# Optimization experiments

Measured on AMD Instinct MI355X. Metric: run time of the kernel, lower is better.

Reference implementation:

```python
import jax, jax.numpy as jnp
import numpy as np

B, S, H, NH, G = 2, 2048, 2048, 16, 2
HD = H // NH          # head_dim = 128
NKV = NH // G         # kv heads = 8
EPS = 1e-6


def setup_inputs() -> dict:
    key = jax.random.key(0)
    ks = jax.random.split(key, 5)
    sc = 0.02
    return {
        "x": jax.random.normal(ks[0], (B, S, H), jnp.float32),
        "wq": jax.random.normal(ks[1], (H, H), jnp.float32) * sc,
        "wk": jax.random.normal(ks[2], (H, H // G), jnp.float32) * sc,
        "wv": jax.random.normal(ks[3], (H, H // G), jnp.float32) * sc,
        "wo": jax.random.normal(ks[4], (H, H), jnp.float32) * sc,
        "rms_w": jnp.ones((HD,), jnp.float32),
        "token_positions": jnp.arange(S, dtype=jnp.int32),
    }


def _rmsnorm(x, w):
    # x: (b, s, HD, n_heads); normalize over the head_dim axis (axis 2)
    ms = jnp.mean(x * x, axis=2, keepdims=True)
    return x * jax.lax.rsqrt(ms + EPS) * w[None, None, :, None]


def _rope(x, pos):
    # x: (b, s, HD, n); interleaved-pair rotation along HD, base 10000
    half = HD // 2
    inv_freq = 1.0 / (10000.0 ** (jnp.arange(half, dtype=jnp.float32) * 2.0 / HD))
    ang = pos.astype(jnp.float32)[:, None] * inv_freq[None, :]   # (s, HD/2)
    cos = jnp.cos(ang)[None, :, :, None]
    sin = jnp.sin(ang)[None, :, :, None]
    x1 = x[:, :, 0::2, :]
    x2 = x[:, :, 1::2, :]
    r1 = x1 * cos - x2 * sin
    r2 = x1 * sin + x2 * cos
    return jnp.stack([r1, r2], axis=3).reshape(x.shape)


def reference(x, wq, wk, wv, wo, rms_w, token_positions):
    b, s, _ = x.shape
    # projections, split hidden as (head_dim, n_heads) exactly like the torch .view
    q = (x @ wq).reshape(b, s, HD, NH)
    k = (x @ wk).reshape(b, s, HD, NKV)
    v = (x @ wv).reshape(b, s, HD, NKV)
    # per-head RMSNorm (over head_dim) then RoPE on Q and K
    q = _rope(_rmsnorm(q, rms_w), token_positions)
    k = _rope(_rmsnorm(k, rms_w), token_positions)
    # grouped-query attention: group G query heads per kv head
    q5 = q.reshape(b, s, HD, NKV, G)
    scores = jnp.einsum('bsdkg,btdk->bkgst', q5, k)          # (b,NKV,G,s,s)
    mask = jnp.triu(jnp.ones((s, s), bool), 1)               # causal
    scores = jnp.where(mask[None, None, None], -jnp.inf, scores)
    attn = jax.nn.softmax(scores / jnp.sqrt(jnp.float32(HD)), axis=-1)
    ctx = jnp.einsum('bkgst,btdk->bkgsd', attn, v)           # (b,NKV,G,s,HD)
    ctx = ctx.reshape(b, NH, s, HD).transpose(0, 2, 1, 3).reshape(b, s, H)
    return ctx @ wo
```

## Files before the change

kernel.cpp:

```cpp
#include <hip/hip_runtime.h>
#include <hip/hip_bf16.h>
#include <stdint.h>

typedef unsigned short u16;
typedef uint32_t u32;
typedef __attribute__((ext_vector_type(8))) short s8v;
typedef __attribute__((ext_vector_type(4))) float f4v;
typedef __attribute__((ext_vector_type(4))) unsigned int u4v;

#define SQ   2048
#define HDIM 2048
#define HD_  128
#define NH_  16
#define NKV_ 8

__device__ __forceinline__ u16 f2b(float f) {
  uint32_t u = __builtin_bit_cast(uint32_t, f);
  u += 0x7fffu + ((u >> 16) & 1u);
  return (u16)(u >> 16);
}
__device__ __forceinline__ float b2f(u16 v) {
  uint32_t u = ((uint32_t)v) << 16;
  return __builtin_bit_cast(float, u);
}
__device__ __forceinline__ u32 pk2(float lo, float hi) {
  return (u32)f2b(lo) | ((u32)f2b(hi) << 16);
}
__device__ __forceinline__ u32 cvtpk(float lo, float hi) {
  u32 r;
  asm("v_cvt_pk_bf16_f32 %0, %1, %2" : "=v"(r) : "v"(lo), "v"(hi));
  return r;
}

__global__ __launch_bounds__(256) void k_cast(const float* __restrict__ in,
                                              u16* __restrict__ out, int n4) {
  int i = blockIdx.x * 256 + threadIdx.x;
  if (i >= n4) return;
  f4v v = *(const f4v*)(in + (size_t)i * 4);
  union { u16 s[4]; uint64_t u; } o;
  o.s[0] = f2b(v[0]); o.s[1] = f2b(v[1]); o.s[2] = f2b(v[2]); o.s[3] = f2b(v[3]);
  *(uint64_t*)(out + (size_t)i * 4) = o.u;
}

__global__ __launch_bounds__(256) void k_transpose4(const float* __restrict__ wq,
                                                    const float* __restrict__ wk,
                                                    const float* __restrict__ wv,
                                                    const float* __restrict__ wo,
                                                    u16* __restrict__ wqt,
                                                    u16* __restrict__ wkt,
                                                    u16* __restrict__ wvt,
                                                    u16* __restrict__ wot) {
  const int z = blockIdx.z;
  const float* in = (z == 0) ? wq : (z == 1) ? wk : (z == 2) ? wv : wo;
  u16* out = (z == 0) ? wqt : (z == 1) ? wkt : (z == 2) ? wvt : wot;
  const int cols = (z == 1 || z == 2) ? 1024 : 2048;
  int c0 = blockIdx.x * 32, r0 = blockIdx.y * 32;
  if (c0 >= cols) return;
  __shared__ float tile[32][33];
  int tx = threadIdx.x & 31, ty = threadIdx.x >> 5;
#pragma unroll
  for (int i = 0; i < 32; i += 8)
    tile[ty + i][tx] = in[(size_t)(r0 + ty + i) * cols + c0 + tx];
  __syncthreads();
#pragma unroll
  for (int i = 0; i < 32; i += 8)
    out[(size_t)(c0 + ty + i) * 2048 + r0 + tx] = f2b(tile[tx][ty + i]);
}

template <int F32OUT>
__global__ __launch_bounds__(256) void k_gemm(const u16* __restrict__ A,
                                              const u16* __restrict__ Bt,
                                              void* __restrict__ C,
                                              int M, int N, int K) {
  __shared__ __align__(16) u16 As[128 * 64];
  __shared__ __align__(16) u16 Bs[128 * 64];
  const int tid = threadIdx.x;
  const int lane = tid & 63, wvi = tid >> 6;
  const int wm = wvi >> 1, wn = wvi & 1;
  const int l15 = lane & 15, l4 = lane >> 4;
  const int m0 = blockIdx.y * 128, n0 = blockIdx.x * 128;
  auto* As3 = (__attribute__((address_space(3))) char*)As;
  auto* Bs3 = (__attribute__((address_space(3))) char*)Bs;
  int srow[4], soff[4];
#pragma unroll
  for (int i = 0; i < 4; i++) {
    int slot = wvi * 4096 + i * 1024 + lane * 16;
    int r = slot >> 7;
    int gc = ((slot >> 4) & 7) ^ (r & 7);
    srow[i] = r; soff[i] = gc * 16;
  }
  f4v acc[4][4] = {};
  for (int k0 = 0; k0 < K; k0 += 64) {
#pragma unroll
    for (int i = 0; i < 4; i++) {
      const char* gA = (const char*)(A + (size_t)(m0 + srow[i]) * K + k0) + soff[i];
      const char* gB = (const char*)(Bt + (size_t)(n0 + srow[i]) * K + k0) + soff[i];
      __builtin_amdgcn_global_load_lds((__attribute__((address_space(1))) void*)gA,
                                       (__attribute__((address_space(3))) void*)(As3 + wvi * 4096 + i * 1024),
                                       16, 0, 0);
      __builtin_amdgcn_global_load_lds((__attribute__((address_space(1))) void*)gB,
                                       (__attribute__((address_space(3))) void*)(Bs3 + wvi * 4096 + i * 1024),
                                       16, 0, 0);
    }
    __syncthreads();
#pragma unroll
    for (int kk = 0; kk < 2; kk++) {
      s8v af[4], bf[4];
#pragma unroll
      for (int i = 0; i < 4; i++) {
        int ra = wm * 64 + i * 16 + l15;
        af[i] = *(const s8v*)((const char*)As + ra * 128 +
                              ((kk * 64 + l4 * 16) ^ ((ra & 7) << 4)));
        int rb = wn * 64 + i * 16 + l15;
        bf[i] = *(const s8v*)((const char*)Bs + rb * 128 +
                              ((kk * 64 + l4 * 16) ^ ((rb & 7) << 4)));
      }
#pragma unroll
      for (int i = 0; i < 4; i++)
#pragma unroll
        for (int j = 0; j < 4; j++)
          acc[i][j] = __builtin_amdgcn_mfma_f32_16x16x32_bf16(af[i], bf[j], acc[i][j], 0, 0, 0);
    }
    __syncthreads();
  }
#pragma unroll
  for (int i = 0; i < 4; i++) {
#pragma unroll
    for (int j = 0; j < 4; j++) {
      int mb = m0 + wm * 64 + i * 16 + l4 * 4;
      int nn = n0 + wn * 64 + j * 16 + l15;
#pragma unroll
      for (int r = 0; r < 4; r++) {
        float v = acc[i][j][r];
        if (F32OUT) ((float*)C)[(size_t)(mb + r) * N + nn] = v;
        else        ((u16*)C)[(size_t)(mb + r) * N + nn]  = f2b(v);
      }
    }
  }
}

__global__ __launch_bounds__(256) void k_normrope(const u16* __restrict__ qkv,
                                                  const float* __restrict__ rms_w,
                                                  const int* __restrict__ pos_arr,
                                                  u16* __restrict__ qq,
                                                  u16* __restrict__ kko,
                                                  u16* __restrict__ vto) {
  int idx = blockIdx.x;
  int b = idx >> 11, s = idx & 2047;
  int t = threadIdx.x;
  __shared__ float part[256];
  __shared__ float rstdq[16], rstdk[8];
  __shared__ float lcos[64], lsin[64];
  float pos = (float)pos_arr[s];
  if (t < 64) {
    float ang = pos * exp2f(-0.20762050593046f * (float)t);
    float sn, cs;
    sincosf(ang, &sn, &cs);
    lcos[t] = cs; lsin[t] = sn;
  }
  const u16* qr = qkv + (size_t)idx * 4096;
  const u16* kr = qr + 2048;
  const u16* vr = qr + 3072;
  int h = t & 15, ch = t >> 4;
  float qv[8]; float ss = 0.f;
#pragma unroll
  for (int j = 0; j < 8; j++) {
    float v = b2f(qr[(ch * 8 + j) * 16 + h]);
    qv[j] = v; ss += v * v;
  }
  part[t] = ss;
  __syncthreads();
  if (t < 16) {
    float tot = 0.f;
#pragma unroll
    for (int c = 0; c < 16; c++) tot += part[c * 16 + t];
    rstdq[t] = rsqrtf(tot * (1.f / 128.f) + 1e-6f);
  }
  __syncthreads();
  {
    float rs = rstdq[h];
    s8v ov;
#pragma unroll
    for (int p = 0; p < 4; p++) {
      int d0 = ch * 8 + p * 2;
      float v0 = qv[p * 2]     * rs * rms_w[d0];
      float v1 = qv[p * 2 + 1] * rs * rms_w[d0 + 1];
      float cs = lcos[d0 >> 1], sn = lsin[d0 >> 1];
      ov[p * 2]     = (short)f2b((v0 * cs - v1 * sn) * 0.08838834764831845f);
      ov[p * 2 + 1] = (short)f2b((v0 * sn + v1 * cs) * 0.08838834764831845f);
    }
    *(s8v*)(qq + ((size_t)(b * 16 + h) * SQ + s) * HD_ + ch * 8) = ov;
  }
  __syncthreads();
  int kv = t & 7, ch2 = t >> 3;
  float kvs[8]; float ssk = 0.f;
  if (t < 128) {
#pragma unroll
    for (int j = 0; j < 8; j++) {
      float v = b2f(kr[(ch2 * 8 + j) * 8 + kv]);
      kvs[j] = v; ssk += v * v;
    }
    part[t] = ssk;
  }
  __syncthreads();
  if (t < 8) {
    float tot = 0.f;
#pragma unroll
    for (int c = 0; c < 16; c++) tot += part[c * 8 + t];
    rstdk[t] = rsqrtf(tot * (1.f / 128.f) + 1e-6f);
  }
  __syncthreads();
  if (t < 128) {
    float rs = rstdk[kv];
    s8v ov;
#pragma unroll
    for (int p = 0; p < 4; p++) {
      int d0 = ch2 * 8 + p * 2;
      float v0 = kvs[p * 2]     * rs * rms_w[d0];
      float v1 = kvs[p * 2 + 1] * rs * rms_w[d0 + 1];
      float cs = lcos[d0 >> 1], sn = lsin[d0 >> 1];
      ov[p * 2]     = (short)f2b(v0 * cs - v1 * sn);
      ov[p * 2 + 1] = (short)f2b(v0 * sn + v1 * cs);
    }
    *(s8v*)(kko + ((size_t)(b * 8 + kv) * SQ + s) * HD_ + ch2 * 8) = ov;
#pragma unroll
    for (int j = 0; j < 8; j++) {
      int d = ch2 * 8 + j;
      vto[((size_t)(b * 8 + kv) * HD_ + d) * SQ + s] = vr[d * 8 + kv];
    }
  }
}

__global__ __launch_bounds__(512, 2) void k_attn(const u16* __restrict__ qq,
                                                 const u16* __restrict__ kk,
                                                 const u16* __restrict__ vt,
                                                 u16* __restrict__ ctx) {
  const int tile = (blockIdx.z == 1) ? (15 - (int)blockIdx.x) : (int)blockIdx.x;
  const int s0 = tile * 128;
  const int h  = blockIdx.y;
  const int b  = blockIdx.z;
  const int kvh = h >> 1;
  const int tid = threadIdx.x, lane = tid & 63, w = tid >> 6;
  const int l15 = lane & 15, l4 = lane >> 4;
  __shared__ __align__(16) u16 Kl[2][64 * 128];
  __shared__ __align__(16) u16 Vl[2][128 * 64];
  auto* K3 = (__attribute__((address_space(3))) char*)&Kl[0][0];
  auto* V3 = (__attribute__((address_space(3))) char*)&Vl[0][0];
  const u16* qbase = qq + (size_t)(b * 16 + h) * SQ * HD_;
  const u16* kbase = kk + (size_t)(b * 8 + kvh) * SQ * HD_;
  const u16* vbase = vt + (size_t)(b * 8 + kvh) * HD_ * SQ;
  const int swp = s0 + w * 16;
  const int mybound = swp + 16;
  const int ntiles = 2 * tile + 2;

  int krow[2], kgo[2], vrow[2], vgo[2];
#pragma unroll
  for (int j = 0; j < 2; j++) {
    int s = j * 8192 + tid * 16;
    krow[j] = s >> 8;
    kgo[j]  = (((s >> 4) & 15) ^ (krow[j] & 7)) * 8;
    vrow[j] = s >> 7;
    vgo[j]  = (((s >> 4) & 7) ^ (vrow[j] & 7)) * 8;
  }

#define STAGE(buf, t0s)                                                           \
  do {                                                                            \
    _Pragma("unroll")                                                             \
    for (int j = 0; j < 2; j++) {                                                 \
      const u16* gk = kbase + (size_t)((t0s) + krow[j]) * HD_ + kgo[j];           \
      __builtin_amdgcn_global_load_lds(                                           \
          (const __attribute__((address_space(1))) void*)gk,                      \
          (__attribute__((address_space(3))) void*)(K3 + (buf) * 16384 + j * 8192 + tid * 16), \
          16, 0, 0);                                                              \
      const u16* gv = vbase + (size_t)vrow[j] * SQ + (t0s) + vgo[j];              \
      __builtin_amdgcn_global_load_lds(                                           \
          (const __attribute__((address_space(1))) void*)gv,                      \
          (__attribute__((address_space(3))) void*)(V3 + (buf) * 16384 + j * 8192 + tid * 16), \
          16, 0, 0);                                                              \
    }                                                                             \
  } while (0)

  s8v qf[4];
#pragma unroll
  for (int c = 0; c < 4; c++)
    qf[c] = *(const s8v*)(qbase + (size_t)(swp + l15) * HD_ + c * 32 + l4 * 8);

  f4v o[8] = {};
  float m2 = -1e30f, l2 = 0.f;

  const int src1 = ((l4 & 1) << 5) + l15;
  const int src2 = src1 + 16;
  const bool selhi = (l4 >> 1) != 0;
  const int swzk = (l15 & 7);

  int xk[4], xv[2];
#pragma unroll
  for (int c = 0; c < 4; c++) xk[c] = ((c * 4 + l4) ^ swzk) * 8;
#pragma unroll
  for (int ks = 0; ks < 2; ks++) xv[ks] = ((ks * 4 + l4) ^ swzk) * 8;

  STAGE(0, 0);
  STAGE(1, 64);
  int cur = 0;
  for (int i = 0; i < ntiles; i++) {
    const int t0 = i * 64;
    asm volatile("s_waitcnt vmcnt(4)" ::: "memory");
    __builtin_amdgcn_s_barrier();
    __builtin_amdgcn_sched_barrier(0);
    if (t0 < mybound) {
      const u16* kb = &Kl[cur][0];
      const u16* vb = &Vl[cur][0];
      f4v sc[4] = {};
      __builtin_amdgcn_s_setprio(1);
#pragma unroll
      for (int tt = 0; tt < 4; tt++) {
        s8v kf0 = *(const s8v*)(kb + (tt * 16 + l15) * 128 + xk[0]);
        s8v kf1 = *(const s8v*)(kb + (tt * 16 + l15) * 128 + xk[1]);
        s8v kf2 = *(const s8v*)(kb + (tt * 16 + l15) * 128 + xk[2]);
        s8v kf3 = *(const s8v*)(kb + (tt * 16 + l15) * 128 + xk[3]);
        sc[tt] = __builtin_amdgcn_mfma_f32_16x16x32_bf16(kf0, qf[0], sc[tt], 0, 0, 0);
        sc[tt] = __builtin_amdgcn_mfma_f32_16x16x32_bf16(kf1, qf[1], sc[tt], 0, 0, 0);
        sc[tt] = __builtin_amdgcn_mfma_f32_16x16x32_bf16(kf2, qf[2], sc[tt], 0, 0, 0);
        sc[tt] = __builtin_amdgcn_mfma_f32_16x16x32_bf16(kf3, qf[3], sc[tt], 0, 0, 0);
      }
      __builtin_amdgcn_s_setprio(0);
      if (t0 + 63 > swp) {
#pragma unroll
        for (int tt = 0; tt < 4; tt++)
#pragma unroll
          for (int r = 0; r < 4; r++) {
            int tg = t0 + tt * 16 + l4 * 4 + r;
            if (tg > swp + l15) sc[tt][r] = -1e30f;
          }
      }
      float mx = sc[0][0];
#pragma unroll
      for (int tt = 0; tt < 4; tt++)
#pragma unroll
        for (int r = 0; r < 4; r++) mx = fmaxf(mx, sc[tt][r]);
      mx = fmaxf(mx, __shfl_xor(mx, 16));
      mx = fmaxf(mx, __shfl_xor(mx, 32));
      if (__any(mx > m2 + 8.f)) {
        float mn = fmaxf(m2, mx);
        float sf = exp2f((m2 - mn) * 1.44269504f);
        m2 = mn; l2 *= sf;
#pragma unroll
        for (int dd = 0; dd < 8; dd++)
#pragma unroll
          for (int r = 0; r < 4; r++) o[dd][r] *= sf;
      }
      u32 pk[4][2];
      float sum = 0.f;
#pragma unroll
      for (int tt = 0; tt < 4; tt++) {
        float p0 = exp2f((sc[tt][0] - m2) * 1.44269504f);
        float p1 = exp2f((sc[tt][1] - m2) * 1.44269504f);
        float p2 = exp2f((sc[tt][2] - m2) * 1.44269504f);
        float p3 = exp2f((sc[tt][3] - m2) * 1.44269504f);
        sum += (p0 + p1) + (p2 + p3);
        pk[tt][0] = cvtpk(p0, p1);
        pk[tt][1] = cvtpk(p2, p3);
      }
      sum += __shfl_xor(sum, 16);
      sum += __shfl_xor(sum, 32);
      l2 += sum;
      s8v pf[2];
#pragma unroll
      for (int ks = 0; ks < 2; ks++) {
        u32 e00 = (u32)__shfl((int)pk[2 * ks][0], src1);
        u32 e01 = (u32)__shfl((int)pk[2 * ks][1], src1);
        u32 e10 = (u32)__shfl((int)pk[2 * ks + 1][0], src1);
        u32 e11 = (u32)__shfl((int)pk[2 * ks + 1][1], src1);
        u32 f00 = (u32)__shfl((int)pk[2 * ks][0], src2);
        u32 f01 = (u32)__shfl((int)pk[2 * ks][1], src2);
        u32 f10 = (u32)__shfl((int)pk[2 * ks + 1][0], src2);
        u32 f11 = (u32)__shfl((int)pk[2 * ks + 1][1], src2);
        u4v fr;
        fr[0] = selhi ? e10 : e00;
        fr[1] = selhi ? e11 : e01;
        fr[2] = selhi ? f10 : f00;
        fr[3] = selhi ? f11 : f01;
        pf[ks] = __builtin_bit_cast(s8v, fr);
      }
      __builtin_amdgcn_s_setprio(1);
#pragma unroll
      for (int dd = 0; dd < 8; dd++) {
        s8v vf0 = *(const s8v*)(vb + (dd * 16 + l15) * 64 + xv[0]);
        s8v vf1 = *(const s8v*)(vb + (dd * 16 + l15) * 64 + xv[1]);
        o[dd] = __builtin_amdgcn_mfma_f32_16x16x32_bf16(vf0, pf[0], o[dd], 0, 0, 0);
        o[dd] = __builtin_amdgcn_mfma_f32_16x16x32_bf16(vf1, pf[1], o[dd], 0, 0, 0);
      }
      __builtin_amdgcn_s_setprio(0);
    }
    __builtin_amdgcn_sched_barrier(0);
    __builtin_amdgcn_s_barrier();
    if (i + 2 < ntiles) STAGE(cur, t0 + 128);
    cur ^= 1;
  }
#undef STAGE
  float inv = 1.f / l2;
  size_t rowoff = ((size_t)(b * SQ + swp + l15)) * HDIM + h * HD_;
#pragma unroll
  for (int dd = 0; dd < 8; dd++) {
    *(u32*)(ctx + rowoff + dd * 16 + l4 * 4)     = cvtpk(o[dd][0] * inv, o[dd][1] * inv);
    *(u32*)(ctx + rowoff + dd * 16 + l4 * 4 + 2) = cvtpk(o[dd][2] * inv, o[dd][3] * inv);
  }
}

extern "C" void kernel_launch(void* const* d_in, const int* in_sizes, int n_in,
                              void* d_out, int out_size, void* d_ws, size_t ws_size,
                              hipStream_t stream) {
  const float* x     = (const float*)d_in[0];
  const float* wq    = (const float*)d_in[1];
  const float* wk    = (const float*)d_in[2];
  const float* wv    = (const float*)d_in[3];
  const float* wo    = (const float*)d_in[4];
  const float* rms_w = (const float*)d_in[5];
  const int*   pos   = (const int*)d_in[6];

  u16* w = (u16*)d_ws;
  u16* xb   = w;
  u16* wqt  = xb   + 8388608;
  u16* wkt  = wqt  + 4194304;
  u16* wvt  = wkt  + 2097152;
  u16* wot  = wvt  + 2097152;
  u16* qkvraw = wot + 4194304;
  u16* kkb  = qkvraw + 16777216;
  u16* vtb  = kkb  + 4194304;
  u16* qqb  = wqt;
  u16* ctxb = xb;

  k_cast<<<8192, 256, 0, stream>>>(x, xb, 2097152);
  k_transpose4<<<dim3(64, 64, 4), 256, 0, stream>>>(wq, wk, wv, wo, wqt, wkt, wvt, wot);

  k_gemm<0><<<dim3(32, 32), 256, 0, stream>>>(xb, wqt, qkvraw, 4096, 4096, 2048);

  k_normrope<<<4096, 256, 0, stream>>>(qkvraw, rms_w, pos, qqb, kkb, vtb);

  k_attn<<<dim3(16, 16, 2), 512, 0, stream>>>(qqb, kkb, vtb, ctxb);

  k_gemm<1><<<dim3(16, 32), 256, 0, stream>>>(ctxb, wot, d_out, 4096, 2048, 2048);
}
```

Before: 270.9 us.

## Add 256x256-tile double-buffered GEMM with direct global-to-LDS loads for QKV projection

Adds a new GEMM kernel for the fused QKV projection. It uses 256x256 output tiles with 8 waves, a two-stage LDS double buffer filled by global_load_lds with an XOR swizzle, explicit vmcnt waits, and raised priority around the MFMA blocks. The larger tile raises arithmetic intensity and cuts global traffic compared with the 128x128 kernel. The cost is only 256 blocks for the 4096x4096 output, which may underfill the device, plus high register and LDS pressure (128 accumulator floats per thread, 128KB of LDS).

```diff
diff --git a/kernel.cpp b/kernel.cpp
--- a/kernel.cpp
+++ b/kernel.cpp
@@ -137,6 +137,107 @@
       }
     }
   }
+}
+
+__global__ __launch_bounds__(512, 2) void k_gemm256(const u16* __restrict__ A,
+                                                    const u16* __restrict__ Bt,
+                                                    u16* __restrict__ C,
+                                                    int M, int N, int K) {
+  __shared__ __align__(16) u16 Al[2][256 * 64];
+  __shared__ __align__(16) u16 Bl[2][256 * 64];
+  const int tid = threadIdx.x;
+  const int lane = tid & 63, wid = tid >> 6;
+  const int wm = wid >> 2, wn = wid & 3;
+  const int l15 = lane & 15, l4 = lane >> 4;
+  const int m0 = blockIdx.y * 256, n0 = blockIdx.x * 256;
+  auto* A3 = (__attribute__((address_space(3))) char*)&Al[0][0];
+  auto* B3 = (__attribute__((address_space(3))) char*)&Bl[0][0];
+  int srow[4], soff[4];
+#pragma unroll
+  for (int j = 0; j < 4; j++) {
+    int slot = j * 8192 + tid * 16;
+    srow[j] = slot >> 7;
+    soff[j] = (((slot >> 4) & 7) ^ (srow[j] & 7)) * 16;
+  }
+  int xk2[2];
+#pragma unroll
+  for (int ks = 0; ks < 2; ks++) xk2[ks] = (((ks * 4 + l4) ^ (l15 & 7)) << 4);
+
+#define STAGE256(buf, k0s)                                                        \
+  do {                                                                            \
+    _Pragma("unroll")                                                             \
+    for (int j = 0; j < 4; j++) {                                                 \
+      const char* gA = (const char*)(A + (size_t)(m0 + srow[j]) * K + (k0s)) + soff[j]; \
+      __builtin_amdgcn_global_load_lds(                                           \
+          (const __attribute__((address_space(1))) void*)gA,                      \
+          (__attribute__((address_space(3))) void*)(A3 + (buf) * 32768 + j * 8192 + tid * 16), \
+          16, 0, 0);                                                              \
+      const char* gB = (const char*)(Bt + (size_t)(n0 + srow[j]) * K + (k0s)) + soff[j]; \
+      __builtin_amdgcn_global_load_lds(                                           \
+          (const __attribute__((address_space(1))) void*)gB,                      \
+          (__attribute__((address_space(3))) void*)(B3 + (buf) * 32768 + j * 8192 + tid * 16), \
+          16, 0, 0);                                                              \
+    }                                                                             \
+  } while (0)
+
+  f4v acc[8][4] = {};
+  STAGE256(0, 0);
+  STAGE256(1, 64);
+  const int nK = K >> 6;
+  for (int t = 0; t < nK; t++) {
+    if (t == nK - 1) asm volatile("s_waitcnt vmcnt(0)" ::: "memory");
+    else             asm volatile("s_waitcnt vmcnt(8)" ::: "memory");
+    __builtin_amdgcn_s_barrier();
+    __builtin_amdgcn_sched_barrier(0);
+    const char* Ab = (const char*)&Al[0][0] + (t & 1) * 32768;
+    const char* Bb = (const char*)&Bl[0][0] + (t & 1) * 32768;
+#pragma unroll
+    for (int qm = 0; qm < 2; qm++)
+#pragma unroll
+      for (int qn = 0; qn < 2; qn++) {
+        s8v af[4][2], bf2[2][2];
+#pragma unroll
+        for (int i2 = 0; i2 < 4; i2++) {
+          int row = wm * 128 + (qm * 4 + i2) * 16 + l15;
+#pragma unroll
+          for (int ks = 0; ks < 2; ks++)
+            af[i2][ks] = *(const s8v*)(Ab + row * 128 + xk2[ks]);
+        }
+#pragma unroll
+        for (int j2 = 0; j2 < 2; j2++) {
+          int row = wn * 64 + (qn * 2 + j2) * 16 + l15;
+#pragma unroll
+          for (int ks = 0; ks < 2; ks++)
+            bf2[j2][ks] = *(const s8v*)(Bb + row * 128 + xk2[ks]);
+        }
+        __builtin_amdgcn_s_setprio(1);
+#pragma unroll
+        for (int i2 = 0; i2 < 4; i2++)
+#pragma unroll
+          for (int j2 = 0; j2 < 2; j2++)
+#pragma unroll
+            for (int ks = 0; ks < 2; ks++)
+              acc[qm * 4 + i2][qn * 2 + j2] = __builtin_amdgcn_mfma_f32_16x16x32_bf16(
+                  af[i2][ks], bf2[j2][ks], acc[qm * 4 + i2][qn * 2 + j2], 0, 0, 0);
+        __builtin_amdgcn_s_setprio(0);
+      }
+    __builtin_amdgcn_sched_barrier(0);
+    if (t + 2 < nK) {
+      __builtin_amdgcn_s_barrier();
+      STAGE256(t & 1, (t + 2) * 64);
+    }
+  }
+#undef STAGE256
+#pragma unroll
+  for (int mi = 0; mi < 8; mi++)
+#pragma unroll
+    for (int ni = 0; ni < 4; ni++) {
+      int mb = m0 + wm * 128 + mi * 16 + l4 * 4;
+      int nn = n0 + wn * 64 + ni * 16 + l15;
+#pragma unroll
+      for (int r = 0; r < 4; r++)
+        C[(size_t)(mb + r) * N + nn] = f2b(acc[mi][ni][r]);
+    }
 }
 
 __global__ __launch_bounds__(256) void k_normrope(const u16* __restrict__ qkv,
@@ -433,7 +534,7 @@
   k_cast<<<8192, 256, 0, stream>>>(x, xb, 2097152);
   k_transpose4<<<dim3(64, 64, 4), 256, 0, stream>>>(wq, wk, wv, wo, wqt, wkt, wvt, wot);
 
-  k_gemm<0><<<dim3(32, 32), 256, 0, stream>>>(xb, wqt, qkvraw, 4096, 4096, 2048);
+  k_gemm256<<<dim3(16, 16), 512, 0, stream>>>(xb, wqt, qkvraw, 4096, 4096, 2048);
 
   k_normrope<<<4096, 256, 0, stream>>>(qkvraw, rms_w, pos, qqb, kkb, vtb);
 
```

After: 250.5 us. 7.5% less time.

## Double-buffer GEMM LDS loads with K=32 stages and smaller output-projection tiles

Applied to the files above, without the earlier changes.

Replaces the single-buffered GEMM with a templated kernel that prefetches two K=32 stages via global_load_lds into double-buffered LDS, uses vmcnt waits instead of a full sync, and raises MFMA priority. Global loads are meant to overlap with MFMA compute. The output projection switches to 64x128 tiles, doubling the block count so more CUs are busy. The attention loop now drains vmcnt fully on its last tile. Costs are more barriers per K step and a new swizzle layout that must stay correct.

```diff
diff --git a/kernel.cpp b/kernel.cpp
--- a/kernel.cpp
+++ b/kernel.cpp
@@ -22,9 +22,6 @@
 __device__ __forceinline__ float b2f(u16 v) {
   uint32_t u = ((uint32_t)v) << 16;
   return __builtin_bit_cast(float, u);
-}
-__device__ __forceinline__ u32 pk2(float lo, float hi) {
-  return (u32)f2b(lo) | ((u32)f2b(hi) << 16);
 }
 __device__ __forceinline__ u32 cvtpk(float lo, float hi) {
   u32 r;
@@ -67,76 +64,106 @@
     out[(size_t)(c0 + ty + i) * 2048 + r0 + tx] = f2b(tile[tx][ty + i]);
 }
 
-template <int F32OUT>
-__global__ __launch_bounds__(256) void k_gemm(const u16* __restrict__ A,
-                                              const u16* __restrict__ Bt,
-                                              void* __restrict__ C,
-                                              int M, int N, int K) {
-  __shared__ __align__(16) u16 As[128 * 64];
-  __shared__ __align__(16) u16 Bs[128 * 64];
+template <int BM, int BN, int F32OUT>
+__global__ __launch_bounds__(256, 4) void k_gemm4w(const u16* __restrict__ A,
+                                                   const u16* __restrict__ Bt,
+                                                   void* __restrict__ C,
+                                                   int M, int N, int K) {
+  constexpr int MF = BM / 32;
+  constexpr int NF = BN / 32;
+  constexpr int NGA = BM / 64;
+  constexpr int NGB = BN / 64;
+  constexpr int NG = NGA + NGB;
+  __shared__ __align__(16) u16 Al[2 * BM * 32];
+  __shared__ __align__(16) u16 Bl[2 * BN * 32];
   const int tid = threadIdx.x;
-  const int lane = tid & 63, wvi = tid >> 6;
-  const int wm = wvi >> 1, wn = wvi & 1;
+  const int lane = tid & 63, wid = tid >> 6;
+  const int wm = wid >> 1, wn = wid & 1;
   const int l15 = lane & 15, l4 = lane >> 4;
-  const int m0 = blockIdx.y * 128, n0 = blockIdx.x * 128;
-  auto* As3 = (__attribute__((address_space(3))) char*)As;
-  auto* Bs3 = (__attribute__((address_space(3))) char*)Bs;
-  int srow[4], soff[4];
-#pragma unroll
-  for (int i = 0; i < 4; i++) {
-    int slot = wvi * 4096 + i * 1024 + lane * 16;
-    int r = slot >> 7;
-    int gc = ((slot >> 4) & 7) ^ (r & 7);
-    srow[i] = r; soff[i] = gc * 16;
-  }
-  f4v acc[4][4] = {};
-  for (int k0 = 0; k0 < K; k0 += 64) {
-#pragma unroll
-    for (int i = 0; i < 4; i++) {
-      const char* gA = (const char*)(A + (size_t)(m0 + srow[i]) * K + k0) + soff[i];
-      const char* gB = (const char*)(Bt + (size_t)(n0 + srow[i]) * K + k0) + soff[i];
-      __builtin_amdgcn_global_load_lds((__attribute__((address_space(1))) void*)gA,
-                                       (__attribute__((address_space(3))) void*)(As3 + wvi * 4096 + i * 1024),
-                                       16, 0, 0);
-      __builtin_amdgcn_global_load_lds((__attribute__((address_space(1))) void*)gB,
-                                       (__attribute__((address_space(3))) void*)(Bs3 + wvi * 4096 + i * 1024),
-                                       16, 0, 0);
-    }
-    __syncthreads();
-#pragma unroll
-    for (int kk = 0; kk < 2; kk++) {
-      s8v af[4], bf[4];
-#pragma unroll
-      for (int i = 0; i < 4; i++) {
-        int ra = wm * 64 + i * 16 + l15;
-        af[i] = *(const s8v*)((const char*)As + ra * 128 +
-                              ((kk * 64 + l4 * 16) ^ ((ra & 7) << 4)));
-        int rb = wn * 64 + i * 16 + l15;
-        bf[i] = *(const s8v*)((const char*)Bs + rb * 128 +
-                              ((kk * 64 + l4 * 16) ^ ((rb & 7) << 4)));
-      }
-#pragma unroll
-      for (int i = 0; i < 4; i++)
-#pragma unroll
-        for (int j = 0; j < 4; j++)
-          acc[i][j] = __builtin_amdgcn_mfma_f32_16x16x32_bf16(af[i], bf[j], acc[i][j], 0, 0, 0);
-    }
-    __syncthreads();
-  }
-#pragma unroll
-  for (int i = 0; i < 4; i++) {
-#pragma unroll
-    for (int j = 0; j < 4; j++) {
-      int mb = m0 + wm * 64 + i * 16 + l4 * 4;
-      int nn = n0 + wn * 64 + j * 16 + l15;
+  const int m0 = blockIdx.y * BM, n0 = blockIdx.x * BN;
+  auto* A3 = (__attribute__((address_space(3))) char*)Al;
+  auto* B3 = (__attribute__((address_space(3))) char*)Bl;
+  const int xoff = ((l4 ^ ((l15 >> 1) & 3)) << 4);
+  int sra[NGA], soa[NGA], srb[NGB], sob[NGB];
+#pragma unroll
+  for (int j = 0; j < NGA; j++) {
+    int s = j * 4096 + tid * 16;
+    sra[j] = s >> 6;
+    soa[j] = ((((s >> 4) & 3) ^ ((s >> 7) & 3)) << 4);
+  }
+#pragma unroll
+  for (int j = 0; j < NGB; j++) {
+    int s = j * 4096 + tid * 16;
+    srb[j] = s >> 6;
+    sob[j] = ((((s >> 4) & 3) ^ ((s >> 7) & 3)) << 4);
+  }
+
+#define STAGE4W(buf, k0s)                                                         \
+  do {                                                                            \
+    _Pragma("unroll")                                                             \
+    for (int j = 0; j < NGA; j++) {                                               \
+      const char* gA = (const char*)(A + (size_t)(m0 + sra[j]) * K + (k0s)) + soa[j]; \
+      __builtin_amdgcn_global_load_lds(                                           \
+          (const __attribute__((address_space(1))) void*)gA,                      \
+          (__attribute__((address_space(3))) void*)(A3 + (buf) * (BM * 64) + j * 4096 + tid * 16), \
+          16, 0, 0);                                                              \
+    }                                                                             \
+    _Pragma("unroll")                                                             \
+    for (int j = 0; j < NGB; j++) {                                               \
+      const char* gB = (const char*)(Bt + (size_t)(n0 + srb[j]) * K + (k0s)) + sob[j]; \
+      __builtin_amdgcn_global_load_lds(                                           \
+          (const __attribute__((address_space(1))) void*)gB,                      \
+          (__attribute__((address_space(3))) void*)(B3 + (buf) * (BN * 64) + j * 4096 + tid * 16), \
+          16, 0, 0);                                                              \
+    }                                                                             \
+  } while (0)
+
+  f4v acc[MF][NF] = {};
+  STAGE4W(0, 0);
+  STAGE4W(1, 32);
+  const int nK = K >> 5;
+  for (int t = 0; t < nK; t++) {
+    if (t == nK - 1)      asm volatile("s_waitcnt vmcnt(0)" ::: "memory");
+    else if (NG == 4)     asm volatile("s_waitcnt vmcnt(4)" ::: "memory");
+    else                  asm volatile("s_waitcnt vmcnt(3)" ::: "memory");
+    __builtin_amdgcn_s_barrier();
+    __builtin_amdgcn_sched_barrier(0);
+    const char* Ab = (const char*)Al + (t & 1) * (BM * 64);
+    const char* Bb = (const char*)Bl + (t & 1) * (BN * 64);
+    s8v af[MF], bf[NF];
+#pragma unroll
+    for (int mi = 0; mi < MF; mi++)
+      af[mi] = *(const s8v*)(Ab + (wm * (BM / 2) + mi * 16 + l15) * 64 + xoff);
+#pragma unroll
+    for (int nj = 0; nj < NF; nj++)
+      bf[nj] = *(const s8v*)(Bb + (wn * (BN / 2) + nj * 16 + l15) * 64 + xoff);
+    __builtin_amdgcn_s_setprio(1);
+#pragma unroll
+    for (int mi = 0; mi < MF; mi++)
+#pragma unroll
+      for (int nj = 0; nj < NF; nj++)
+        acc[mi][nj] = __builtin_amdgcn_mfma_f32_16x16x32_bf16(af[mi], bf[nj], acc[mi][nj], 0, 0, 0);
+    __builtin_amdgcn_s_setprio(0);
+    __builtin_amdgcn_sched_barrier(0);
+    if (t + 2 < nK) {
+      __builtin_amdgcn_s_barrier();
+      STAGE4W(t & 1, (t + 2) * 32);
+    }
+  }
+#undef STAGE4W
+#pragma unroll
+  for (int mi = 0; mi < MF; mi++)
+#pragma unroll
+    for (int nj = 0; nj < NF; nj++) {
+      int mb = m0 + wm * (BM / 2) + mi * 16 + l4 * 4;
+      int nn = n0 + wn * (BN / 2) + nj * 16 + l15;
 #pragma unroll
       for (int r = 0; r < 4; r++) {
-        float v = acc[i][j][r];
+        float v = acc[mi][nj][r];
         if (F32OUT) ((float*)C)[(size_t)(mb + r) * N + nn] = v;
         else        ((u16*)C)[(size_t)(mb + r) * N + nn]  = f2b(v);
       }
     }
-  }
 }
 
 __global__ __launch_bounds__(256) void k_normrope(const u16* __restrict__ qkv,
@@ -304,7 +331,8 @@
   int cur = 0;
   for (int i = 0; i < ntiles; i++) {
     const int t0 = i * 64;
-    asm volatile("s_waitcnt vmcnt(4)" ::: "memory");
+    if (i == ntiles - 1) asm volatile("s_waitcnt vmcnt(0)" ::: "memory");
+    else                 asm volatile("s_waitcnt vmcnt(4)" ::: "memory");
     __builtin_amdgcn_s_barrier();
     __builtin_amdgcn_sched_barrier(0);
     if (t0 < mybound) {
@@ -433,11 +461,11 @@
   k_cast<<<8192, 256, 0, stream>>>(x, xb, 2097152);
   k_transpose4<<<dim3(64, 64, 4), 256, 0, stream>>>(wq, wk, wv, wo, wqt, wkt, wvt, wot);
 
-  k_gemm<0><<<dim3(32, 32), 256, 0, stream>>>(xb, wqt, qkvraw, 4096, 4096, 2048);
+  k_gemm4w<128, 128, 0><<<dim3(32, 32), 256, 0, stream>>>(xb, wqt, qkvraw, 4096, 4096, 2048);
 
   k_normrope<<<4096, 256, 0, stream>>>(qkvraw, rms_w, pos, qqb, kkb, vtb);
 
   k_attn<<<dim3(16, 16, 2), 512, 0, stream>>>(qqb, kkb, vtb, ctxb);
 
-  k_gemm<1><<<dim3(16, 32), 256, 0, stream>>>(ctxb, wot, d_out, 4096, 2048, 2048);
-}
+  k_gemm4w<64, 128, 1><<<dim3(16, 64), 256, 0, stream>>>(ctxb, wot, d_out, 4096, 2048, 2048);
+}
```

After: 272.4 us. About the same (+0.5%).

## Add 256x256 double-buffered QKV GEMM and XCD-aware block remapping

Applied to the files above, without the earlier changes.

Replaces the 128x128 QKV projection GEMM with a new 256x256-tile, 512-thread kernel. It double-buffers LDS and splits each K-step into four quadrant phases so prefetch loads overlap MFMA work. Both GEMMs and the attention kernel remap block indices so neighbouring tiles or heads land on the same XCD, aiming for better L2 reuse. The attention loop also waits for all loads on its final tile. The larger tile raises LDS and register pressure and cuts the grid to 256 blocks, which may limit occupancy.

```diff
diff --git a/kernel.cpp b/kernel.cpp
--- a/kernel.cpp
+++ b/kernel.cpp
@@ -22,9 +22,6 @@
 __device__ __forceinline__ float b2f(u16 v) {
   uint32_t u = ((uint32_t)v) << 16;
   return __builtin_bit_cast(float, u);
-}
-__device__ __forceinline__ u32 pk2(float lo, float hi) {
-  return (u32)f2b(lo) | ((u32)f2b(hi) << 16);
 }
 __device__ __forceinline__ u32 cvtpk(float lo, float hi) {
   u32 r;
@@ -78,7 +75,10 @@
   const int lane = tid & 63, wvi = tid >> 6;
   const int wm = wvi >> 1, wn = wvi & 1;
   const int l15 = lane & 15, l4 = lane >> 4;
-  const int m0 = blockIdx.y * 128, n0 = blockIdx.x * 128;
+  const int f = blockIdx.y * gridDim.x + blockIdx.x;
+  const int cpx = (gridDim.x * gridDim.y) >> 3;
+  const int swz = (f & 7) * cpx + (f >> 3);
+  const int m0 = (swz / gridDim.x) * 128, n0 = (swz % gridDim.x) * 128;
   auto* As3 = (__attribute__((address_space(3))) char*)As;
   auto* Bs3 = (__attribute__((address_space(3))) char*)Bs;
   int srow[4], soff[4];
@@ -137,6 +137,125 @@
       }
     }
   }
+}
+
+__global__ __launch_bounds__(512, 2) void k_gemm256(const u16* __restrict__ A,
+                                                    const u16* __restrict__ Bt,
+                                                    u16* __restrict__ C,
+                                                    int M, int N, int K) {
+  __shared__ __align__(16) u16 Al[2 * 256 * 64];
+  __shared__ __align__(16) u16 Bl[2 * 256 * 64];
+  const int tid = threadIdx.x;
+  const int lane = tid & 63, wid = tid >> 6;
+  const int wm = wid >> 2, wn = wid & 3;
+  const int l15 = lane & 15, l4 = lane >> 4;
+  const int f = blockIdx.y * gridDim.x + blockIdx.x;
+  const int cpx = (gridDim.x * gridDim.y) >> 3;
+  const int swz = (f & 7) * cpx + (f >> 3);
+  const int m0 = (swz / gridDim.x) * 256, n0 = (swz % gridDim.x) * 256;
+  auto* A3 = (__attribute__((address_space(3))) char*)Al;
+  auto* B3 = (__attribute__((address_space(3))) char*)Bl;
+  const int r0s = tid >> 3, chs = tid & 7;
+  const int gco = ((chs ^ (r0s & 7)) << 4);
+  int xk2[2];
+#pragma unroll
+  for (int ks = 0; ks < 2; ks++) xk2[ks] = (((ks * 4 + l4) ^ (l15 & 7)) << 4);
+
+#define SA(buf, kt, h)                                                            \
+  do {                                                                            \
+    _Pragma("unroll")                                                             \
+    for (int c = 0; c < 2; c++) {                                                 \
+      const char* g = (const char*)(A + (size_t)(m0 + (h) * 128 + c * 64 + r0s) * K + (kt) * 64) + gco; \
+      __builtin_amdgcn_global_load_lds(                                           \
+          (const __attribute__((address_space(1))) void*)g,                       \
+          (__attribute__((address_space(3))) void*)(A3 + (buf) * 32768 + (h) * 16384 + c * 8192 + tid * 16), \
+          16, 0, 0);                                                              \
+    }                                                                             \
+  } while (0)
+#define SB(buf, kt, h)                                                            \
+  do {                                                                            \
+    _Pragma("unroll")                                                             \
+    for (int c = 0; c < 2; c++) {                                                 \
+      const char* g = (const char*)(Bt + (size_t)(n0 + (h) * 128 + c * 64 + r0s) * K + (kt) * 64) + gco; \
+      __builtin_amdgcn_global_load_lds(                                           \
+          (const __attribute__((address_space(1))) void*)g,                       \
+          (__attribute__((address_space(3))) void*)(B3 + (buf) * 32768 + (h) * 16384 + c * 8192 + tid * 16), \
+          16, 0, 0);                                                              \
+    }                                                                             \
+  } while (0)
+
+#define PHASE(QM, QN, bufc, STAGE_STMT)                                           \
+  do {                                                                            \
+    const char* Ab = (const char*)Al + (bufc) * 32768;                            \
+    const char* Bb = (const char*)Bl + (bufc) * 32768;                            \
+    s8v af[4][2], bf[2][2];                                                       \
+    _Pragma("unroll")                                                             \
+    for (int i2 = 0; i2 < 4; i2++) {                                              \
+      int row = (QM) * 128 + wm * 64 + i2 * 16 + l15;                             \
+      _Pragma("unroll")                                                           \
+      for (int ks = 0; ks < 2; ks++)                                              \
+        af[i2][ks] = *(const s8v*)(Ab + row * 128 + xk2[ks]);                     \
+    }                                                                             \
+    _Pragma("unroll")                                                             \
+    for (int j2 = 0; j2 < 2; j2++) {                                              \
+      int row = (QN) * 128 + wn * 32 + j2 * 16 + l15;                             \
+      _Pragma("unroll")                                                           \
+      for (int ks = 0; ks < 2; ks++)                                              \
+        bf[j2][ks] = *(const s8v*)(Bb + row * 128 + xk2[ks]);                     \
+    }                                                                             \
+    STAGE_STMT;                                                                   \
+    __builtin_amdgcn_s_barrier();                                                 \
+    asm volatile("s_waitcnt lgkmcnt(0)" ::: "memory");                            \
+    __builtin_amdgcn_sched_barrier(0);                                            \
+    __builtin_amdgcn_s_setprio(1);                                                \
+    _Pragma("unroll")                                                             \
+    for (int i2 = 0; i2 < 4; i2++)                                                \
+      _Pragma("unroll")                                                           \
+      for (int j2 = 0; j2 < 2; j2++)                                              \
+        _Pragma("unroll")                                                         \
+        for (int ks = 0; ks < 2; ks++)                                            \
+          acc[(QM) * 4 + i2][(QN) * 2 + j2] = __builtin_amdgcn_mfma_f32_16x16x32_bf16( \
+              af[i2][ks], bf[j2][ks], acc[(QM) * 4 + i2][(QN) * 2 + j2], 0, 0, 0); \
+    __builtin_amdgcn_s_setprio(0);                                                \
+    __builtin_amdgcn_sched_barrier(0);                                            \
+    __builtin_amdgcn_s_barrier();                                                 \
+  } while (0)
+
+  f4v acc[8][4] = {};
+  SA(0, 0, 0); SB(0, 0, 0); SA(0, 0, 1); SB(0, 0, 1);
+  SA(1, 1, 0); SB(1, 1, 0);
+  const int nT = K >> 6;
+  for (int it = 0;; it++) {
+    const int T0 = 2 * it;
+    const bool last = (T0 + 2 >= nT);
+    asm volatile("s_waitcnt vmcnt(4)" ::: "memory");
+    __builtin_amdgcn_s_barrier();
+    PHASE(0, 0, 0, SA(1, T0 + 1, 1));
+    PHASE(0, 1, 0, SB(1, T0 + 1, 1));
+    PHASE(1, 0, 0, { if (!last) SA(0, T0 + 2, 0); });
+    PHASE(1, 1, 0, { if (!last) SB(0, T0 + 2, 0); });
+    if (last) asm volatile("s_waitcnt vmcnt(0)" ::: "memory");
+    else      asm volatile("s_waitcnt vmcnt(4)" ::: "memory");
+    __builtin_amdgcn_s_barrier();
+    PHASE(0, 0, 1, { if (!last) SA(0, T0 + 2, 1); });
+    PHASE(0, 1, 1, { if (!last) SB(0, T0 + 2, 1); });
+    PHASE(1, 0, 1, { if (!last) SA(1, T0 + 3, 0); });
+    PHASE(1, 1, 1, { if (!last) SB(1, T0 + 3, 0); });
+    if (last) break;
+  }
+#undef PHASE
+#undef SA
+#undef SB
+#pragma unroll
+  for (int mi = 0; mi < 8; mi++)
+#pragma unroll
+    for (int ni = 0; ni < 4; ni++) {
+      int mb = m0 + (mi >> 2) * 128 + wm * 64 + (mi & 3) * 16 + l4 * 4;
+      int nn = n0 + (ni >> 1) * 128 + wn * 32 + (ni & 1) * 16 + l15;
+#pragma unroll
+      for (int r = 0; r < 4; r++)
+        C[(size_t)(mb + r) * N + nn] = f2b(acc[mi][ni][r]);
+    }
 }
 
 __global__ __launch_bounds__(256) void k_normrope(const u16* __restrict__ qkv,
@@ -235,10 +354,14 @@
                                                  const u16* __restrict__ kk,
                                                  const u16* __restrict__ vt,
                                                  u16* __restrict__ ctx) {
-  const int tile = (blockIdx.z == 1) ? (15 - (int)blockIdx.x) : (int)blockIdx.x;
+  const int f   = (int)blockIdx.z * 256 + (int)blockIdx.y * 16 + (int)blockIdx.x;
+  const int xcd = f & 7;
+  const int wix = f >> 3;
+  const int b    = wix >> 5;
+  const int h    = xcd * 2 + ((wix >> 4) & 1);
+  const int x    = wix & 15;
+  const int tile = (b == 1) ? (15 - x) : x;
   const int s0 = tile * 128;
-  const int h  = blockIdx.y;
-  const int b  = blockIdx.z;
   const int kvh = h >> 1;
   const int tid = threadIdx.x, lane = tid & 63, w = tid >> 6;
   const int l15 = lane & 15, l4 = lane >> 4;
@@ -304,7 +427,8 @@
   int cur = 0;
   for (int i = 0; i < ntiles; i++) {
     const int t0 = i * 64;
-    asm volatile("s_waitcnt vmcnt(4)" ::: "memory");
+    if (i == ntiles - 1) asm volatile("s_waitcnt vmcnt(0)" ::: "memory");
+    else                 asm volatile("s_waitcnt vmcnt(4)" ::: "memory");
     __builtin_amdgcn_s_barrier();
     __builtin_amdgcn_sched_barrier(0);
     if (t0 < mybound) {
@@ -433,7 +557,7 @@
   k_cast<<<8192, 256, 0, stream>>>(x, xb, 2097152);
   k_transpose4<<<dim3(64, 64, 4), 256, 0, stream>>>(wq, wk, wv, wo, wqt, wkt, wvt, wot);
 
-  k_gemm<0><<<dim3(32, 32), 256, 0, stream>>>(xb, wqt, qkvraw, 4096, 4096, 2048);
+  k_gemm256<<<dim3(16, 16), 512, 0, stream>>>(xb, wqt, qkvraw, 4096, 4096, 2048);
 
   k_normrope<<<4096, 256, 0, stream>>>(qkvraw, rms_w, pos, qqb, kkb, vtb);
 
```

Result: faster. 255.1 us (-5.8%).
